# Performance work log

Measured on AMD Instinct MI355X. Metric: run time of the kernel, lower is better.

Reference implementation:

```python
import jax, jax.numpy as jnp
import numpy as np

N_NODES = 10000
N_EDGES = 320000
HIDDEN = 16      # hidden_state_size
MSG = 64         # message_size
EDGE_FEAT = 32


def setup_inputs() -> dict:
    key = jax.random.key(0)
    ks = jax.random.split(key, 8)
    node_features = jax.random.normal(ks[0], (N_NODES, HIDDEN), dtype=jnp.float32)
    edge_features = jax.random.normal(ks[1], (N_EDGES, EDGE_FEAT), dtype=jnp.float32)
    edge_sources = jax.random.randint(ks[2], (N_EDGES,), 0, N_NODES, dtype=jnp.int32)
    edge_targets = jax.random.randint(ks[3], (N_EDGES,), 0, N_NODES, dtype=jnp.int32)
    hidden = jax.random.normal(ks[4], (N_NODES, HIDDEN), dtype=jnp.float32)
    initial = jax.random.normal(ks[5], (N_NODES, HIDDEN), dtype=jnp.float32)
    # Dense(edge_feat -> MSG*HIDDEN), glorot-ish scale
    W = jax.random.normal(ks[6], (EDGE_FEAT, MSG * HIDDEN), dtype=jnp.float32) / np.float32(np.sqrt(EDGE_FEAT))
    b = jnp.zeros((MSG * HIDDEN,), dtype=jnp.float32)
    return {
        "node_features": node_features,
        "edge_features": edge_features,
        "edge_sources": edge_sources,
        "edge_targets": edge_targets,
        "hidden": hidden,
        "initial": initial,
        "W": W,
        "b": b,
    }


def reference(node_features, edge_features, edge_sources, edge_targets, hidden, initial, W, b):
    # Per edge: edge_mat = Dense(edge_feat) reshaped (MSG, HIDDEN);
    # message = edge_mat @ hidden[source]; aggregate = sum over incoming edges per target node.
    num_nodes = node_features.shape[0]
    edge_mat = (edge_features @ W + b).reshape(-1, MSG, HIDDEN)  # [E, M, H]
    neigh = hidden[edge_sources]                                  # [E, H] gather
    messages = jnp.einsum("emh,eh->em", edge_mat, neigh)         # [E, M] batched matvec
    out = jax.ops.segment_sum(messages, edge_targets, num_segments=num_nodes)  # [N, M]
    return out
```

## Files before the change

### kernel.cpp

```cpp
#include <hip/hip_runtime.h>
#include <hip/hip_bf16.h>

#define N_NODES 10000
#define N_EDGES 320000
#define HIDDEN 16
#define MSG 64
#define EDGE_FEAT 32
#define KSTEPS 17
#define EPB 128

typedef __attribute__((ext_vector_type(2))) _Float16 f16x2;
typedef __attribute__((ext_vector_type(4))) _Float16 f16x4;
typedef __attribute__((ext_vector_type(8))) _Float16 f16x8;
typedef __attribute__((ext_vector_type(4))) float    f32x4;

union H8 { f16x8 v; f16x2 p[4]; f16x4 q[2]; };

__global__ void zero_prep(const float* __restrict__ W, const float* __restrict__ bias,
                          ushort* __restrict__ WrB, int* __restrict__ cnt,
                          float4* __restrict__ out4, int n4) {
    if (blockIdx.x < KSTEPS) {
        const int ks   = blockIdx.x;
        const int nt   = threadIdx.x >> 6;
        const int lane = threadIdx.x & 63;
        const int g    = lane >> 4;
        const int n    = nt * 16 + (lane & 15);
        ushort* dst = WrB + (((size_t)ks * 4 + nt) * 64 + lane) * 8;
        #pragma unroll
        for (int i = 0; i < 8; ++i) {
            const int k = ks * 32 + g * 8 + i;
            float v;
            if (k < 512)      v = W[(size_t)(k >> 4) * 1024 + n * 16 + (k & 15)];
            else if (k < 528) v = bias[n * 16 + (k - 512)];
            else              v = 0.0f;
            const _Float16 hv = (_Float16)v;
            dst[i] = *reinterpret_cast<const ushort*>(&hv);
        }
    } else if (blockIdx.x < KSTEPS + 40) {
        const int idx = (blockIdx.x - KSTEPS) * 256 + threadIdx.x;
        if (idx < N_NODES) cnt[idx] = 0;
    } else {
        const int i = (blockIdx.x - KSTEPS - 40) * 256 + threadIdx.x;
        if (i < n4) out4[i] = make_float4(0.f, 0.f, 0.f, 0.f);
    }
}

__global__ __launch_bounds__(256) void rank_kernel(const int* __restrict__ tgt,
                                                   int* __restrict__ cnt,
                                                   int* __restrict__ rank) {
    const int e = blockIdx.x * 256 + threadIdx.x;
    if (e < N_EDGES) rank[e] = atomicAdd(&cnt[tgt[e]], 1);
}

__global__ __launch_bounds__(1024) void scan_kernel(const int* __restrict__ cnt,
                                                    int* __restrict__ starts) {
    __shared__ int wsum[16];
    __shared__ int wbase[16];
    const int tid  = threadIdx.x;
    const int lane = tid & 63;
    const int wv   = tid >> 6;
    int c[10];
    int s = 0;
    #pragma unroll
    for (int j = 0; j < 10; ++j) {
        const int idx = tid * 10 + j;
        c[j] = (idx < N_NODES) ? cnt[idx] : 0;
        s += c[j];
    }
    int v = s;
    #pragma unroll
    for (int d = 1; d < 64; d <<= 1) {
        const int u = __shfl_up(v, d);
        if (lane >= d) v += u;
    }
    if (lane == 63) wsum[wv] = v;
    __syncthreads();
    if (tid < 16) {
        const int w = wsum[tid];
        int iv = w;
        #pragma unroll
        for (int d = 1; d < 16; d <<= 1) {
            const int u = __shfl_up(iv, d);
            if (tid >= d) iv += u;
        }
        wbase[tid] = iv - w;
    }
    __syncthreads();
    int running = wbase[wv] + (v - s);
    #pragma unroll
    for (int j = 0; j < 10; ++j) {
        const int idx = tid * 10 + j;
        if (idx < N_NODES) starts[idx] = running;
        running += c[j];
    }
    if (tid == 1023) starts[N_NODES] = N_EDGES;
}

__global__ __launch_bounds__(256) void build_iperm(
    const int* __restrict__ tgt, const int* __restrict__ rank,
    const int* __restrict__ starts, int* __restrict__ iperm) {
    const int e = blockIdx.x * 256 + threadIdx.x;
    if (e < N_EDGES) iperm[starts[tgt[e]] + rank[e]] = e;
}

__global__ __launch_bounds__(256) void fused_msg(
    const int*    __restrict__ iperm,
    const int*    __restrict__ tgt,
    const int*    __restrict__ src,
    const float*  __restrict__ ef,
    const float*  __restrict__ hidden,
    const ushort* __restrict__ WrB,
    float*        __restrict__ out)
{
    __shared__ _Float16 ef_h[EPB][36];
    __shared__ _Float16 nb_h[EPB][16];
    __shared__ int      tgt_s[EPB];
    __shared__ float    msg_s[EPB][68];

    const int tid = threadIdx.x;
    const int s0  = blockIdx.x * EPB;

    {
        const int sl   = tid >> 1;
        const int half = tid & 1;
        const int e    = iperm[s0 + sl];
        const int sn   = src[e];

        const float4* ep = (const float4*)(ef + (size_t)e * EDGE_FEAT + half * 16);
        const float4 v0 = ep[0], v1 = ep[1], v2 = ep[2], v3 = ep[3];
        _Float16* dst = &ef_h[sl][half * 16];
        *(f16x4*)(dst + 0)  = f16x4{(_Float16)v0.x, (_Float16)v0.y, (_Float16)v0.z, (_Float16)v0.w};
        *(f16x4*)(dst + 4)  = f16x4{(_Float16)v1.x, (_Float16)v1.y, (_Float16)v1.z, (_Float16)v1.w};
        *(f16x4*)(dst + 8)  = f16x4{(_Float16)v2.x, (_Float16)v2.y, (_Float16)v2.z, (_Float16)v2.w};
        *(f16x4*)(dst + 12) = f16x4{(_Float16)v3.x, (_Float16)v3.y, (_Float16)v3.z, (_Float16)v3.w};

        const float4* hp = (const float4*)(hidden + (size_t)sn * HIDDEN + half * 8);
        const float4 h0 = hp[0], h1 = hp[1];
        *(f16x8*)&nb_h[sl][half * 8] =
            f16x8{(_Float16)h0.x, (_Float16)h0.y, (_Float16)h0.z, (_Float16)h0.w,
                  (_Float16)h1.x, (_Float16)h1.y, (_Float16)h1.z, (_Float16)h1.w};

        if (half) {
            ef_h[sl][32] = (_Float16)1.0f;
            ef_h[sl][33] = (_Float16)0.0f;
            ef_h[sl][34] = (_Float16)0.0f;
            ef_h[sl][35] = (_Float16)0.0f;
        } else {
            tgt_s[sl] = tgt[e];
        }
    }
    __syncthreads();

    const int wave = tid >> 6;
    const int lane = tid & 63;
    const int er   = lane & 15;
    const int g    = lane >> 4;
    const int eA   = wave * 32 + er;
    const int eB   = eA + 16;
    const int hoff = (g & 1) * 8;
    const int fg   = g >> 1;

    H8 nbA, nbB;
    nbA.v = *(const f16x8*)&nb_h[eA][hoff];
    nbB.v = *(const f16x8*)&nb_h[eB][hoff];

    f32x4 aA0 = {0.f,0.f,0.f,0.f}, aA1 = aA0, aA2 = aA0, aA3 = aA0;
    f32x4 aB0 = aA0, aB1 = aA0, aB2 = aA0, aB3 = aA0;
    const f16x8* Bp = (const f16x8*)WrB;

    #pragma unroll
    for (int ks = 0; ks < KSTEPS; ++ks) {
        const f16x8 b0 = Bp[(ks * 4 + 0) * 64 + lane];
        const f16x8 b1 = Bp[(ks * 4 + 1) * 64 + lane];
        const f16x8 b2 = Bp[(ks * 4 + 2) * 64 + lane];
        const f16x8 b3 = Bp[(ks * 4 + 3) * 64 + lane];

        const _Float16 a_A = ef_h[eA][2 * ks + fg];
        const _Float16 a_B = ef_h[eB][2 * ks + fg];
        const f16x2 avA = {a_A, a_A};
        const f16x2 avB = {a_B, a_B};
        H8 afA, afB;
        #pragma unroll
        for (int q = 0; q < 4; ++q) {
            afA.p[q] = avA * nbA.p[q];
            afB.p[q] = avB * nbB.p[q];
        }
        aA0 = __builtin_amdgcn_mfma_f32_16x16x32_f16(afA.v, b0, aA0, 0, 0, 0);
        aA1 = __builtin_amdgcn_mfma_f32_16x16x32_f16(afA.v, b1, aA1, 0, 0, 0);
        aA2 = __builtin_amdgcn_mfma_f32_16x16x32_f16(afA.v, b2, aA2, 0, 0, 0);
        aA3 = __builtin_amdgcn_mfma_f32_16x16x32_f16(afA.v, b3, aA3, 0, 0, 0);
        aB0 = __builtin_amdgcn_mfma_f32_16x16x32_f16(afB.v, b0, aB0, 0, 0, 0);
        aB1 = __builtin_amdgcn_mfma_f32_16x16x32_f16(afB.v, b1, aB1, 0, 0, 0);
        aB2 = __builtin_amdgcn_mfma_f32_16x16x32_f16(afB.v, b2, aB2, 0, 0, 0);
        aB3 = __builtin_amdgcn_mfma_f32_16x16x32_f16(afB.v, b3, aB3, 0, 0, 0);
    }

    #pragma unroll
    for (int r = 0; r < 4; ++r) {
        const int rowA = wave * 32 + g * 4 + r;
        msg_s[rowA][ 0 + er] = aA0[r];
        msg_s[rowA][16 + er] = aA1[r];
        msg_s[rowA][32 + er] = aA2[r];
        msg_s[rowA][48 + er] = aA3[r];
        const int rowB = rowA + 16;
        msg_s[rowB][ 0 + er] = aB0[r];
        msg_s[rowB][16 + er] = aB1[r];
        msg_s[rowB][32 + er] = aB2[r];
        msg_s[rowB][48 + er] = aB3[r];
    }
    __syncthreads();

    const int c = tid & 63;
    const int rbase = (tid >> 6) * 32;
    float run = msg_s[rbase][c];
    int   cur = tgt_s[rbase];
    #pragma unroll
    for (int r = 1; r < 32; ++r) {
        const int   tg = tgt_s[rbase + r];
        const float m  = msg_s[rbase + r][c];
        if (tg != cur) {
            atomicAdd(out + (size_t)cur * MSG + c, run);
            cur = tg;
            run = m;
        } else {
            run += m;
        }
    }
    atomicAdd(out + (size_t)cur * MSG + c, run);
}

__global__ __launch_bounds__(256) void zero_out(float* __restrict__ p, int n4) {
    const int i = blockIdx.x * 256 + threadIdx.x;
    if (i < n4) ((float4*)p)[i] = make_float4(0.f, 0.f, 0.f, 0.f);
}

__global__ __launch_bounds__(256, 4) void msg_mfma(
    const float* __restrict__ ef, const int* __restrict__ src,
    const int* __restrict__ tgt, const float* __restrict__ hidden,
    const ushort* __restrict__ WrB, float* __restrict__ out)
{
    __shared__ float ef_s[64][36];
    __shared__ float neigh_s[64][20];
    __shared__ int   tgt_s[64];
    const int tid = threadIdx.x;
    const int e0  = blockIdx.x * 64;
    {
        const int e = tid >> 2, h4 = (tid & 3) * 4;
        const int s = src[e0 + e];
        *(float4*)&neigh_s[e][h4] = *(const float4*)(hidden + (size_t)s * HIDDEN + h4);
    }
    {
        const int e = tid >> 2, f8 = (tid & 3) * 8;
        const float* p = ef + (size_t)(e0 + e) * EDGE_FEAT + f8;
        *(float4*)&ef_s[e][f8]     = *(const float4*)(p);
        *(float4*)&ef_s[e][f8 + 4] = *(const float4*)(p + 4);
    }
    if (tid < 64) { ef_s[tid][32] = 1.0f; ef_s[tid][33] = 0.0f; tgt_s[tid] = tgt[e0 + tid]; }
    __syncthreads();
    const int wave = tid >> 6, lane = tid & 63;
    const int er = lane & 15, g = lane >> 4;
    const int e_loc = wave * 16 + er;
    const int h0 = (g & 1) * 8, fg = g >> 1;
    float nb[8];
    #pragma unroll
    for (int j = 0; j < 8; ++j) nb[j] = neigh_s[e_loc][h0 + j];
    f32x4 acc0 = {0.f,0.f,0.f,0.f}, acc1 = acc0, acc2 = acc0, acc3 = acc0;
    const f16x8* Bp = (const f16x8*)WrB;
    #pragma unroll
    for (int ks = 0; ks < KSTEPS; ++ks) {
        const float a = ef_s[e_loc][2 * ks + fg];
        f16x8 af;
        #pragma unroll
        for (int j = 0; j < 8; ++j) af[j] = (_Float16)(a * nb[j]);
        const f16x8 b0 = Bp[(ks * 4 + 0) * 64 + lane];
        const f16x8 b1 = Bp[(ks * 4 + 1) * 64 + lane];
        const f16x8 b2 = Bp[(ks * 4 + 2) * 64 + lane];
        const f16x8 b3 = Bp[(ks * 4 + 3) * 64 + lane];
        acc0 = __builtin_amdgcn_mfma_f32_16x16x32_f16(af, b0, acc0, 0, 0, 0);
        acc1 = __builtin_amdgcn_mfma_f32_16x16x32_f16(af, b1, acc1, 0, 0, 0);
        acc2 = __builtin_amdgcn_mfma_f32_16x16x32_f16(af, b2, acc2, 0, 0, 0);
        acc3 = __builtin_amdgcn_mfma_f32_16x16x32_f16(af, b3, acc3, 0, 0, 0);
    }
    #pragma unroll
    for (int r = 0; r < 4; ++r) {
        const int t = tgt_s[wave * 16 + g * 4 + r];
        float* op = out + (size_t)t * MSG;
        atomicAdd(op +      er, acc0[r]);
        atomicAdd(op + 16 + er, acc1[r]);
        atomicAdd(op + 32 + er, acc2[r]);
        atomicAdd(op + 48 + er, acc3[r]);
    }
}

extern "C" void kernel_launch(void* const* d_in, const int* in_sizes, int n_in,
                              void* d_out, int out_size, void* d_ws, size_t ws_size,
                              hipStream_t stream) {
    const float* ef     = (const float*)d_in[1];
    const int*   src    = (const int*)d_in[2];
    const int*   tgt    = (const int*)d_in[3];
    const float* hidden = (const float*)d_in[4];
    const float* W      = (const float*)d_in[6];
    const float* bias   = (const float*)d_in[7];
    float* out = (float*)d_out;
    char*  ws  = (char*)d_ws;

    const size_t o_wrb    = 0;
    const size_t o_starts = 69632;
    const size_t o_cnt    = 109648;
    const size_t o_rank   = 149648;
    const size_t o_iperm  = 1429648;
    const size_t need     = o_iperm + 1280000;

    ushort* WrB = (ushort*)(ws + o_wrb);
    const int n4 = out_size / 4;

    if (ws_size >= need) {
        int* starts = (int*)(ws + o_starts);
        int* cnt    = (int*)(ws + o_cnt);
        int* rank   = (int*)(ws + o_rank);
        int* iperm  = (int*)(ws + o_iperm);

        const int zb_cnt = 40;
        const int zb_out = (n4 + 255) / 256;
        zero_prep<<<KSTEPS + zb_cnt + zb_out, 256, 0, stream>>>(W, bias, WrB, cnt,
                                                                (float4*)out, n4);
        rank_kernel<<<(N_EDGES + 255) / 256, 256, 0, stream>>>(tgt, cnt, rank);
        scan_kernel<<<1, 1024, 0, stream>>>(cnt, starts);
        build_iperm<<<(N_EDGES + 255) / 256, 256, 0, stream>>>(tgt, rank, starts, iperm);
        fused_msg<<<N_EDGES / EPB, 256, 0, stream>>>(iperm, tgt, src, ef, hidden, WrB, out);
    } else {
        zero_prep<<<KSTEPS, 256, 0, stream>>>(W, bias, WrB, nullptr, nullptr, 0);
        zero_out<<<(n4 + 255) / 256, 256, 0, stream>>>(out, n4);
        msg_mfma<<<N_EDGES / 64, 256, 0, stream>>>(ef, src, tgt, hidden, WrB, out);
    }
}
```

Measured before the change: 85.83 us.

## Pack sorted edge descriptors and store messages in fp16 shared memory

The permutation kernel now writes a packed int4 descriptor (edge id, source, target) at each edge's sorted slot. The fused message kernel then reads one coalesced 16-byte record instead of chasing iperm, src and tgt with dependent random loads. The message staging buffer in shared memory becomes fp16, halving LDS use, and launch bounds request 5 blocks per SM for higher occupancy. In exchange, the scatter writes 16 bytes per edge instead of 4, and messages are rounded to fp16 before the per-target reduction.

```diff
diff --git a/kernel.cpp b/kernel.cpp
--- a/kernel.cpp
+++ b/kernel.cpp
@@ -96,17 +96,19 @@
     if (tid == 1023) starts[N_NODES] = N_EDGES;
 }
 
-__global__ __launch_bounds__(256) void build_iperm(
+__global__ __launch_bounds__(256) void build_desc(
     const int* __restrict__ tgt, const int* __restrict__ rank,
-    const int* __restrict__ starts, int* __restrict__ iperm) {
+    const int* __restrict__ starts, const int* __restrict__ src,
+    int4* __restrict__ edesc) {
     const int e = blockIdx.x * 256 + threadIdx.x;
-    if (e < N_EDGES) iperm[starts[tgt[e]] + rank[e]] = e;
-}
-
-__global__ __launch_bounds__(256) void fused_msg(
-    const int*    __restrict__ iperm,
-    const int*    __restrict__ tgt,
-    const int*    __restrict__ src,
+    if (e < N_EDGES) {
+        const int t = tgt[e];
+        edesc[starts[t] + rank[e]] = make_int4(e, src[e], t, 0);
+    }
+}
+
+__global__ __launch_bounds__(256, 5) void fused_msg(
+    const int4*   __restrict__ edesc,
     const float*  __restrict__ ef,
     const float*  __restrict__ hidden,
     const ushort* __restrict__ WrB,
@@ -115,38 +117,39 @@
     __shared__ _Float16 ef_h[EPB][36];
     __shared__ _Float16 nb_h[EPB][16];
     __shared__ int      tgt_s[EPB];
-    __shared__ float    msg_s[EPB][68];
+    __shared__ _Float16 msg_h[EPB][68];
 
     const int tid = threadIdx.x;
     const int s0  = blockIdx.x * EPB;
 
     {
-        const int sl   = tid >> 1;
-        const int half = tid & 1;
-        const int e    = iperm[s0 + sl];
-        const int sn   = src[e];
-
-        const float4* ep = (const float4*)(ef + (size_t)e * EDGE_FEAT + half * 16);
+        const int sl = tid >> 1;
+        const int hf = tid & 1;
+        const int4 d = edesc[s0 + sl];
+        const int e  = d.x;
+        const int sn = d.y;
+
+        const float4* ep = (const float4*)(ef + (size_t)e * EDGE_FEAT + hf * 16);
         const float4 v0 = ep[0], v1 = ep[1], v2 = ep[2], v3 = ep[3];
-        _Float16* dst = &ef_h[sl][half * 16];
+        _Float16* dst = &ef_h[sl][hf * 16];
         *(f16x4*)(dst + 0)  = f16x4{(_Float16)v0.x, (_Float16)v0.y, (_Float16)v0.z, (_Float16)v0.w};
         *(f16x4*)(dst + 4)  = f16x4{(_Float16)v1.x, (_Float16)v1.y, (_Float16)v1.z, (_Float16)v1.w};
         *(f16x4*)(dst + 8)  = f16x4{(_Float16)v2.x, (_Float16)v2.y, (_Float16)v2.z, (_Float16)v2.w};
         *(f16x4*)(dst + 12) = f16x4{(_Float16)v3.x, (_Float16)v3.y, (_Float16)v3.z, (_Float16)v3.w};
 
-        const float4* hp = (const float4*)(hidden + (size_t)sn * HIDDEN + half * 8);
+        const float4* hp = (const float4*)(hidden + (size_t)sn * HIDDEN + hf * 8);
         const float4 h0 = hp[0], h1 = hp[1];
-        *(f16x8*)&nb_h[sl][half * 8] =
+        *(f16x8*)&nb_h[sl][hf * 8] =
             f16x8{(_Float16)h0.x, (_Float16)h0.y, (_Float16)h0.z, (_Float16)h0.w,
                   (_Float16)h1.x, (_Float16)h1.y, (_Float16)h1.z, (_Float16)h1.w};
 
-        if (half) {
+        if (hf) {
             ef_h[sl][32] = (_Float16)1.0f;
             ef_h[sl][33] = (_Float16)0.0f;
             ef_h[sl][34] = (_Float16)0.0f;
             ef_h[sl][35] = (_Float16)0.0f;
         } else {
-            tgt_s[sl] = tgt[e];
+            tgt_s[sl] = d.z;
         }
     }
     __syncthreads();
@@ -198,26 +201,26 @@
     #pragma unroll
     for (int r = 0; r < 4; ++r) {
         const int rowA = wave * 32 + g * 4 + r;
-        msg_s[rowA][ 0 + er] = aA0[r];
-        msg_s[rowA][16 + er] = aA1[r];
-        msg_s[rowA][32 + er] = aA2[r];
-        msg_s[rowA][48 + er] = aA3[r];
+        msg_h[rowA][ 0 + er] = (_Float16)aA0[r];
+        msg_h[rowA][16 + er] = (_Float16)aA1[r];
+        msg_h[rowA][32 + er] = (_Float16)aA2[r];
+        msg_h[rowA][48 + er] = (_Float16)aA3[r];
         const int rowB = rowA + 16;
-        msg_s[rowB][ 0 + er] = aB0[r];
-        msg_s[rowB][16 + er] = aB1[r];
-        msg_s[rowB][32 + er] = aB2[r];
-        msg_s[rowB][48 + er] = aB3[r];
+        msg_h[rowB][ 0 + er] = (_Float16)aB0[r];
+        msg_h[rowB][16 + er] = (_Float16)aB1[r];
+        msg_h[rowB][32 + er] = (_Float16)aB2[r];
+        msg_h[rowB][48 + er] = (_Float16)aB3[r];
     }
     __syncthreads();
 
     const int c = tid & 63;
     const int rbase = (tid >> 6) * 32;
-    float run = msg_s[rbase][c];
+    float run = (float)msg_h[rbase][c];
     int   cur = tgt_s[rbase];
     #pragma unroll
     for (int r = 1; r < 32; ++r) {
         const int   tg = tgt_s[rbase + r];
-        const float m  = msg_s[rbase + r][c];
+        const float m  = (float)msg_h[rbase + r][c];
         if (tg != cur) {
             atomicAdd(out + (size_t)cur * MSG + c, run);
             cur = tg;
@@ -308,17 +311,17 @@
     const size_t o_starts = 69632;
     const size_t o_cnt    = 109648;
     const size_t o_rank   = 149648;
-    const size_t o_iperm  = 1429648;
-    const size_t need     = o_iperm + 1280000;
+    const size_t o_desc   = 1429648;
+    const size_t need     = o_desc + (size_t)N_EDGES * 16;
 
     ushort* WrB = (ushort*)(ws + o_wrb);
     const int n4 = out_size / 4;
 
     if (ws_size >= need) {
-        int* starts = (int*)(ws + o_starts);
-        int* cnt    = (int*)(ws + o_cnt);
-        int* rank   = (int*)(ws + o_rank);
-        int* iperm  = (int*)(ws + o_iperm);
+        int*  starts = (int*)(ws + o_starts);
+        int*  cnt    = (int*)(ws + o_cnt);
+        int*  rank   = (int*)(ws + o_rank);
+        int4* edesc  = (int4*)(ws + o_desc);
 
         const int zb_cnt = 40;
         const int zb_out = (n4 + 255) / 256;
@@ -326,8 +329,8 @@
                                                                 (float4*)out, n4);
         rank_kernel<<<(N_EDGES + 255) / 256, 256, 0, stream>>>(tgt, cnt, rank);
         scan_kernel<<<1, 1024, 0, stream>>>(cnt, starts);
-        build_iperm<<<(N_EDGES + 255) / 256, 256, 0, stream>>>(tgt, rank, starts, iperm);
-        fused_msg<<<N_EDGES / EPB, 256, 0, stream>>>(iperm, tgt, src, ef, hidden, WrB, out);
+        build_desc<<<(N_EDGES + 255) / 256, 256, 0, stream>>>(tgt, rank, starts, src, edesc);
+        fused_msg<<<N_EDGES / EPB, 256, 0, stream>>>(edesc, ef, hidden, WrB, out);
     } else {
         zero_prep<<<KSTEPS, 256, 0, stream>>>(W, bias, WrB, nullptr, nullptr, 0);
         zero_out<<<(n4 + 255) / 256, 256, 0, stream>>>(out, n4);
```

Result: faster. 76.64 us (-10.7%).
